# Kernel tuning notes

Hardware: AMD Instinct MI355X
Metric: run time of the kernel (lower is better)

Reference implementation:

```python
import jax, jax.numpy as jnp
import numpy as np

EPS = 1e-6
DN = ('NCHW', 'OIHW', 'NCHW')


def _dw_conv(s, w, dilation, k):
    pad = dilation * (k - 1) // 2
    return jax.lax.conv_general_dilated(
        s, w, window_strides=(1, 1), padding=[(pad, pad), (pad, pad)],
        rhs_dilation=(dilation, dilation), dimension_numbers=DN,
        feature_group_count=4)


def _branch(s, dw_w, pw_w, pw_b, dilation, k):
    h = _dw_conv(s, dw_w, dilation, k)           # [B,4,H,W]
    # pointwise 1x1 conv 4 -> 1
    return jnp.einsum('bchw,oc->bohw', h, pw_w) + pw_b[None, :, None, None]


def setup_inputs() -> dict:
    key = jax.random.key(0)
    ks = jax.random.split(key, 12)
    B, C, H, W = 32, 64, 128, 128
    nb, rh = 3, 8
    d = {}
    d['x'] = jax.random.normal(ks[0], (B, C, H, W), dtype=jnp.float32)
    # branch 0: k=3 d=1; branch 1: k=7 d=1; branch 2: k=7 d=2
    d['dw0'] = jax.random.normal(ks[1], (4, 1, 3, 3), dtype=jnp.float32) * 0.2
    d['dw1'] = jax.random.normal(ks[2], (4, 1, 7, 7), dtype=jnp.float32) * 0.1
    d['dw2'] = jax.random.normal(ks[3], (4, 1, 7, 7), dtype=jnp.float32) * 0.1
    d['pw0_w'] = jax.random.normal(ks[4], (1, 4), dtype=jnp.float32) * 0.5
    d['pw0_b'] = jnp.zeros((1,), dtype=jnp.float32)
    d['pw1_w'] = jax.random.normal(ks[5], (1, 4), dtype=jnp.float32) * 0.5
    d['pw1_b'] = jnp.zeros((1,), dtype=jnp.float32)
    d['pw2_w'] = jax.random.normal(ks[6], (1, 4), dtype=jnp.float32) * 0.5
    d['pw2_b'] = jnp.zeros((1,), dtype=jnp.float32)
    # router: 1x1 convs on pooled [B,4,1,1] == dense layers
    d['rw1'] = jax.random.normal(ks[7], (rh, 4), dtype=jnp.float32) * 0.5
    d['rb1'] = jnp.zeros((rh,), dtype=jnp.float32)
    d['rw2'] = jax.random.normal(ks[8], (nb, rh), dtype=jnp.float32) * 0.3
    d['rb2'] = jnp.zeros((nb,), dtype=jnp.float32)
    # t_raw = softplus_inverse(1.0)
    d['t_raw'] = jnp.asarray(np.log(np.expm1(1.0)), dtype=jnp.float32)
    return d


def reference(x, dw0, dw1, dw2, pw0_w, pw0_b, pw1_w, pw1_b, pw2_w, pw2_b,
              rw1, rb1, rw2, rb2, t_raw):
    B, C, H, W = x.shape
    avg_map = jnp.mean(x, axis=1, keepdims=True)        # [B,1,H,W]
    max_map = jnp.max(x, axis=1, keepdims=True)         # [B,1,H,W]
    xs = jnp.linspace(-1.0, 1.0, W, dtype=x.dtype)
    ys = jnp.linspace(-1.0, 1.0, H, dtype=x.dtype)
    yy, xx = jnp.meshgrid(ys, xs, indexing='ij')
    xg = jnp.broadcast_to(xx[None, None], (B, 1, H, W))
    yg = jnp.broadcast_to(yy[None, None], (B, 1, H, W))
    s = jnp.concatenate([avg_map, max_map, xg, yg], axis=1)  # [B,4,H,W]

    # router: global avg pool -> 1x1 conv -> relu -> 1x1 conv -> softmax
    pooled = jnp.mean(s, axis=(2, 3))                    # [B,4]
    hid = jax.nn.relu(pooled @ rw1.T + rb1)              # [B,rh]
    logits = hid @ rw2.T + rb2                           # [B,nb]
    rw = jax.nn.softmax(logits, axis=1)                  # [B,nb]

    z = jnp.stack([
        _branch(s, dw0, pw0_w, pw0_b, 1, 3),
        _branch(s, dw1, pw1_w, pw1_b, 1, 7),
        _branch(s, dw2, pw2_w, pw2_b, 2, 7),
    ], axis=1)                                           # [B,nb,1,H,W]

    wlogits = jnp.sum(rw[:, :, None, None, None] * z, axis=1)  # [B,1,H,W]
    T = jax.nn.softplus(t_raw) + EPS
    sa = jax.nn.sigmoid(wlogits / T)                     # [B,1,H,W]
    Y = x * sa                                           # [B,C,H,W]
    return (Y, sa)
```

## Files before the change

### kernel.cpp

```cpp
#include <hip/hip_runtime.h>

#define B_ 32
#define C_ 64
#define H_ 128
#define W_ 128
#define HW_ (H_*W_)
#define CHW_ (C_*HW_)

typedef float f4 __attribute__((ext_vector_type(4)));

__global__ __launch_bounds__(256) void k0_zpos(
    const float* __restrict__ dw0, const float* __restrict__ dw1,
    const float* __restrict__ dw2,
    const float* __restrict__ pw0w, const float* __restrict__ pw0b,
    const float* __restrict__ pw1w, const float* __restrict__ pw1b,
    const float* __restrict__ pw2w, const float* __restrict__ pw2b,
    float* __restrict__ zpos)
{
    int p = blockIdx.x * 256 + threadIdx.x;
    int gy = p >> 7, gx = p & 127;
    const float sc = 2.0f / 127.0f;
    float z0 = pw0b[0], z1 = pw1b[0], z2 = pw2b[0];
    float px0 = pw0w[2], py0 = pw0w[3];
    float px1 = pw1w[2], py1 = pw1w[3];
    float px2 = pw2w[2], py2 = pw2w[3];

    #pragma unroll
    for (int ky = 0; ky < 3; ++ky)
    #pragma unroll
    for (int kx = 0; kx < 3; ++kx) {
        int iy = gy + ky - 1, ix = gx + kx - 1;
        bool ok = ((unsigned)iy < H_) && ((unsigned)ix < W_);
        float xv = ok ? ix * sc - 1.0f : 0.0f;
        float yv = ok ? iy * sc - 1.0f : 0.0f;
        int t = ky * 3 + kx;
        z0 += px0 * dw0[18 + t] * xv + py0 * dw0[27 + t] * yv;
    }
    #pragma unroll
    for (int ky = 0; ky < 7; ++ky)
    #pragma unroll
    for (int kx = 0; kx < 7; ++kx) {
        int iy = gy + ky - 3, ix = gx + kx - 3;
        bool ok = ((unsigned)iy < H_) && ((unsigned)ix < W_);
        float xv = ok ? ix * sc - 1.0f : 0.0f;
        float yv = ok ? iy * sc - 1.0f : 0.0f;
        int t = ky * 7 + kx;
        z1 += px1 * dw1[98 + t] * xv + py1 * dw1[147 + t] * yv;
    }
    #pragma unroll
    for (int ky = 0; ky < 7; ++ky)
    #pragma unroll
    for (int kx = 0; kx < 7; ++kx) {
        int iy = gy + (ky - 3) * 2, ix = gx + (kx - 3) * 2;
        bool ok = ((unsigned)iy < H_) && ((unsigned)ix < W_);
        float xv = ok ? ix * sc - 1.0f : 0.0f;
        float yv = ok ? iy * sc - 1.0f : 0.0f;
        int t = ky * 7 + kx;
        z2 += px2 * dw2[98 + t] * xv + py2 * dw2[147 + t] * yv;
    }
    zpos[p]           = z0;
    zpos[HW_ + p]     = z1;
    zpos[2 * HW_ + p] = z2;
}

__global__ __launch_bounds__(256) void k1_reduce(
    const float* __restrict__ x, float* __restrict__ avgmap,
    float* __restrict__ maxmap, float* __restrict__ partial)
{
    int t = blockIdx.x * 256 + threadIdx.x;
    int base = t * 4;
    int b = base >> 14;
    int q = base & (HW_ - 1);
    const float4* xp = (const float4*)(x + (size_t)b * CHW_ + q);
    float4 v = xp[0];
    float4 s = v, m = v;
    #pragma unroll 8
    for (int c = 1; c < C_; ++c) {
        float4 u = xp[c * (HW_ / 4)];
        s.x += u.x; s.y += u.y; s.z += u.z; s.w += u.w;
        m.x = fmaxf(m.x, u.x); m.y = fmaxf(m.y, u.y);
        m.z = fmaxf(m.z, u.z); m.w = fmaxf(m.w, u.w);
    }
    const float inv = 1.0f / C_;
    float4 a = make_float4(s.x * inv, s.y * inv, s.z * inv, s.w * inv);
    ((float4*)avgmap)[t] = a;
    ((float4*)maxmap)[t] = m;

    float la = a.x + a.y + a.z + a.w;
    float lm = m.x + m.y + m.z + m.w;
    #pragma unroll
    for (int o = 32; o > 0; o >>= 1) {
        la += __shfl_down(la, o);
        lm += __shfl_down(lm, o);
    }
    __shared__ float wa[4], wm[4];
    int lane = threadIdx.x & 63, wid = threadIdx.x >> 6;
    if (lane == 0) { wa[wid] = la; wm[wid] = lm; }
    __syncthreads();
    if (threadIdx.x == 0) {
        partial[2 * blockIdx.x]     = wa[0] + wa[1] + wa[2] + wa[3];
        partial[2 * blockIdx.x + 1] = wm[0] + wm[1] + wm[2] + wm[3];
    }
}

__global__ void k2_router(const float* __restrict__ partial,
                          const float* __restrict__ rw1, const float* __restrict__ rb1,
                          const float* __restrict__ rw2, const float* __restrict__ rb2,
                          const float* __restrict__ t_raw,
                          float* __restrict__ rwout)
{
    int b = threadIdx.x;
    if (b >= B_) return;
    if (b == 0)
        rwout[96] = 1.0f / (log1pf(expf(t_raw[0])) + 1e-6f);
    float s0 = 0.0f, s1 = 0.0f;
    #pragma unroll
    for (int i = 0; i < 16; ++i) {
        s0 += partial[2 * (b * 16 + i)];
        s1 += partial[2 * (b * 16 + i) + 1];
    }
    float p0 = s0 * (1.0f / HW_);
    float p1 = s1 * (1.0f / HW_);
    float hid[8];
    #pragma unroll
    for (int j = 0; j < 8; ++j)
        hid[j] = fmaxf(0.0f, rb1[j] + rw1[j * 4] * p0 + rw1[j * 4 + 1] * p1);
    float lg[3];
    #pragma unroll
    for (int i = 0; i < 3; ++i) {
        float acc = rb2[i];
        #pragma unroll
        for (int j = 0; j < 8; ++j) acc += hid[j] * rw2[i * 8 + j];
        lg[i] = acc;
    }
    float mx = fmaxf(lg[0], fmaxf(lg[1], lg[2]));
    float e0 = expf(lg[0] - mx), e1 = expf(lg[1] - mx), e2 = expf(lg[2] - mx);
    float inv = 1.0f / (e0 + e1 + e2);
    rwout[b * 3 + 0] = e0 * inv;
    rwout[b * 3 + 1] = e1 * inv;
    rwout[b * 3 + 2] = e2 * inv;
}

__global__ __launch_bounds__(256) void k3_conv(
    const float* __restrict__ avgmap, const float* __restrict__ maxmap,
    const float* __restrict__ dw0, const float* __restrict__ dw1,
    const float* __restrict__ dw2,
    const float* __restrict__ pw0w, const float* __restrict__ pw1w,
    const float* __restrict__ pw2w,
    const float* __restrict__ zpos, const float* __restrict__ rw,
    float* __restrict__ sa_out)
{
    __shared__ float sA[14][140];
    __shared__ float sM[14][140];
    __shared__ float wA0[9], wM0[9];
    __shared__ float wA1[49], wM1[49], wA2[49], wM2[49];

    int b  = blockIdx.y;
    int y0 = blockIdx.x * 2;
    int tix = threadIdx.x;
    const float* am = avgmap + (size_t)b * HW_;
    const float* mm = maxmap + (size_t)b * HW_;

    for (int idx = tix; idx < 14 * 32; idx += 256) {
        int r = idx >> 5, c4 = idx & 31;
        int gy = y0 - 6 + r;
        bool ok = (unsigned)gy < H_;
        float4 av = ok ? ((const float4*)(am + gy * W_))[c4]
                       : make_float4(0.f, 0.f, 0.f, 0.f);
        float4 mv = ok ? ((const float4*)(mm + gy * W_))[c4]
                       : make_float4(0.f, 0.f, 0.f, 0.f);
        float* pa = &sA[r][6 + c4 * 4];
        float* pm = &sM[r][6 + c4 * 4];
        pa[0] = av.x; pa[1] = av.y; pa[2] = av.z; pa[3] = av.w;
        pm[0] = mv.x; pm[1] = mv.y; pm[2] = mv.z; pm[3] = mv.w;
    }
    for (int idx = tix; idx < 14 * 12; idx += 256) {
        int r = idx / 12, c = idx % 12;
        int cc = (c < 6) ? c : (134 + c - 6);
        sA[r][cc] = 0.0f;
        sM[r][cc] = 0.0f;
    }
    if (tix < 9)  { wA0[tix] = pw0w[0] * dw0[tix];
                    wM0[tix] = pw0w[1] * dw0[9 + tix]; }
    if (tix < 49) { wA1[tix] = pw1w[0] * dw1[tix];
                    wM1[tix] = pw1w[1] * dw1[49 + tix];
                    wA2[tix] = pw2w[0] * dw2[tix];
                    wM2[tix] = pw2w[1] * dw2[49 + tix]; }
    __syncthreads();

    int ly = tix >> 7;
    int lx = tix & 127;
    int gy = y0 + ly;
    int pidx = gy * W_ + lx;

    float z0 = zpos[pidx];
    float z1 = zpos[HW_ + pidx];
    float z2 = zpos[2 * HW_ + pidx];

    #pragma unroll
    for (int ky = 0; ky < 7; ++ky) {
        const float* ra = &sA[ly + 3 + ky][lx + 3];
        const float* rm = &sM[ly + 3 + ky][lx + 3];
        float av[7], mv[7];
        #pragma unroll
        for (int j = 0; j < 7; ++j) { av[j] = ra[j]; mv[j] = rm[j]; }
        #pragma unroll
        for (int j = 0; j < 7; ++j) {
            int t = ky * 7 + j;
            z1 += wA1[t] * av[j] + wM1[t] * mv[j];
        }
        if (ky >= 2 && ky <= 4) {
            #pragma unroll
            for (int j = 2; j <= 4; ++j) {
                int t = (ky - 2) * 3 + (j - 2);
                z0 += wA0[t] * av[j] + wM0[t] * mv[j];
            }
        }
    }
    #pragma unroll
    for (int ky = 0; ky < 7; ++ky) {
        const float* ra = &sA[ly + 2 * ky][lx];
        const float* rm = &sM[ly + 2 * ky][lx];
        #pragma unroll
        for (int kx = 0; kx < 7; ++kx) {
            int t = ky * 7 + kx;
            z2 += wA2[t] * ra[2 * kx] + wM2[t] * rm[2 * kx];
        }
    }

    float wl = rw[b * 3] * z0 + rw[b * 3 + 1] * z1 + rw[b * 3 + 2] * z2;
    float s = 1.0f / (1.0f + expf(-wl * rw[96]));
    sa_out[(size_t)b * HW_ + pidx] = s;
}

__global__ __launch_bounds__(256) void k4_apply(
    const float* __restrict__ x, const float* __restrict__ sa,
    float* __restrict__ y)
{
    int tile = blockIdx.x;
    int cg   = blockIdx.y;
    int b  = tile >> 4;
    int p4 = (tile & 15) * 256 + threadIdx.x;

    f4 sv = ((const f4*)(sa + (size_t)b * HW_))[p4];
    const f4* xb = (const f4*)(x + (size_t)b * CHW_) + p4;
    f4*       yb = (f4*)(y + (size_t)b * CHW_) + p4;

    #pragma unroll 4
    for (int k = 0; k < 16; ++k) {
        int c = cg * 16 + k;
        f4 v = xb[c * (HW_ / 4)];
        f4 r = v * sv;
        __builtin_nontemporal_store(r, &yb[c * (HW_ / 4)]);
    }
}

extern "C" void kernel_launch(void* const* d_in, const int* in_sizes, int n_in,
                              void* d_out, int out_size, void* d_ws, size_t ws_size,
                              hipStream_t stream)
{
    const float* x     = (const float*)d_in[0];
    const float* dw0   = (const float*)d_in[1];
    const float* dw1   = (const float*)d_in[2];
    const float* dw2   = (const float*)d_in[3];
    const float* pw0w  = (const float*)d_in[4];
    const float* pw0b  = (const float*)d_in[5];
    const float* pw1w  = (const float*)d_in[6];
    const float* pw1b  = (const float*)d_in[7];
    const float* pw2w  = (const float*)d_in[8];
    const float* pw2b  = (const float*)d_in[9];
    const float* rw1   = (const float*)d_in[10];
    const float* rb1   = (const float*)d_in[11];
    const float* rw2   = (const float*)d_in[12];
    const float* rb2   = (const float*)d_in[13];
    const float* t_raw = (const float*)d_in[14];

    float* ws      = (float*)d_ws;
    float* avgmap  = ws;
    float* maxmap  = ws + 524288;
    float* partial = ws + 1048576;
    float* rw      = ws + 1049600;
    float* zpos    = ws + 1049728;

    float* Y  = (float*)d_out;
    float* sa = Y + (size_t)B_ * CHW_;

    k0_zpos<<<HW_ / 256, 256, 0, stream>>>(
        dw0, dw1, dw2, pw0w, pw0b, pw1w, pw1b, pw2w, pw2b, zpos);
    k1_reduce<<<B_ * HW_ / 4 / 256, 256, 0, stream>>>(x, avgmap, maxmap, partial);
    k2_router<<<1, 64, 0, stream>>>(partial, rw1, rb1, rw2, rb2, t_raw, rw);

    dim3 g3(H_ / 2, B_);
    k3_conv<<<g3, 256, 0, stream>>>(
        avgmap, maxmap, dw0, dw1, dw2, pw0w, pw1w, pw2w, zpos, rw, sa);

    dim3 g4(B_ * HW_ / 4 / 256, 4);
    k4_apply<<<g4, 256, 0, stream>>>(x, sa, Y);
}
```

Before: 320.1 us.

## Fuse router, conv and apply kernels into one per-tile kernel

```diff
diff --git a/kernel.cpp b/kernel.cpp
--- a/kernel.cpp
+++ b/kernel.cpp
@@ -103,57 +103,26 @@
     }
 }
 
-__global__ void k2_router(const float* __restrict__ partial,
-                          const float* __restrict__ rw1, const float* __restrict__ rb1,
-                          const float* __restrict__ rw2, const float* __restrict__ rb2,
-                          const float* __restrict__ t_raw,
-                          float* __restrict__ rwout)
-{
-    int b = threadIdx.x;
-    if (b >= B_) return;
-    if (b == 0)
-        rwout[96] = 1.0f / (log1pf(expf(t_raw[0])) + 1e-6f);
-    float s0 = 0.0f, s1 = 0.0f;
-    #pragma unroll
-    for (int i = 0; i < 16; ++i) {
-        s0 += partial[2 * (b * 16 + i)];
-        s1 += partial[2 * (b * 16 + i) + 1];
-    }
-    float p0 = s0 * (1.0f / HW_);
-    float p1 = s1 * (1.0f / HW_);
-    float hid[8];
-    #pragma unroll
-    for (int j = 0; j < 8; ++j)
-        hid[j] = fmaxf(0.0f, rb1[j] + rw1[j * 4] * p0 + rw1[j * 4 + 1] * p1);
-    float lg[3];
-    #pragma unroll
-    for (int i = 0; i < 3; ++i) {
-        float acc = rb2[i];
-        #pragma unroll
-        for (int j = 0; j < 8; ++j) acc += hid[j] * rw2[i * 8 + j];
-        lg[i] = acc;
-    }
-    float mx = fmaxf(lg[0], fmaxf(lg[1], lg[2]));
-    float e0 = expf(lg[0] - mx), e1 = expf(lg[1] - mx), e2 = expf(lg[2] - mx);
-    float inv = 1.0f / (e0 + e1 + e2);
-    rwout[b * 3 + 0] = e0 * inv;
-    rwout[b * 3 + 1] = e1 * inv;
-    rwout[b * 3 + 2] = e2 * inv;
-}
-
-__global__ __launch_bounds__(256) void k3_conv(
+__global__ __launch_bounds__(256) void k34_fused(
+    const float* __restrict__ x,
     const float* __restrict__ avgmap, const float* __restrict__ maxmap,
     const float* __restrict__ dw0, const float* __restrict__ dw1,
     const float* __restrict__ dw2,
     const float* __restrict__ pw0w, const float* __restrict__ pw1w,
     const float* __restrict__ pw2w,
-    const float* __restrict__ zpos, const float* __restrict__ rw,
-    float* __restrict__ sa_out)
+    const float* __restrict__ zpos,
+    const float* __restrict__ partial,
+    const float* __restrict__ rw1, const float* __restrict__ rb1,
+    const float* __restrict__ rw2, const float* __restrict__ rb2,
+    const float* __restrict__ t_raw,
+    float* __restrict__ y, float* __restrict__ sa_out)
 {
     __shared__ float sA[14][140];
     __shared__ float sM[14][140];
     __shared__ float wA0[9], wM0[9];
     __shared__ float wA1[49], wM1[49], wA2[49], wM2[49];
+    __shared__ __align__(16) float ssa[256];
+    __shared__ float sRW[4];
 
     int b  = blockIdx.y;
     int y0 = blockIdx.x * 2;
@@ -186,6 +155,35 @@
                     wM1[tix] = pw1w[1] * dw1[49 + tix];
                     wA2[tix] = pw2w[0] * dw2[tix];
                     wM2[tix] = pw2w[1] * dw2[49 + tix]; }
+    if (tix == 0) {
+        float s0 = 0.0f, s1 = 0.0f;
+        #pragma unroll
+        for (int i = 0; i < 16; ++i) {
+            s0 += partial[2 * (b * 16 + i)];
+            s1 += partial[2 * (b * 16 + i) + 1];
+        }
+        float p0 = s0 * (1.0f / HW_);
+        float p1 = s1 * (1.0f / HW_);
+        float hid[8];
+        #pragma unroll
+        for (int j = 0; j < 8; ++j)
+            hid[j] = fmaxf(0.0f, rb1[j] + rw1[j * 4] * p0 + rw1[j * 4 + 1] * p1);
+        float lg[3];
+        #pragma unroll
+        for (int i = 0; i < 3; ++i) {
+            float acc = rb2[i];
+            #pragma unroll
+            for (int j = 0; j < 8; ++j) acc += hid[j] * rw2[i * 8 + j];
+            lg[i] = acc;
+        }
+        float mx = fmaxf(lg[0], fmaxf(lg[1], lg[2]));
+        float e0 = expf(lg[0] - mx), e1 = expf(lg[1] - mx), e2 = expf(lg[2] - mx);
+        float inv = 1.0f / (e0 + e1 + e2);
+        sRW[0] = e0 * inv;
+        sRW[1] = e1 * inv;
+        sRW[2] = e2 * inv;
+        sRW[3] = 1.0f / (log1pf(expf(t_raw[0])) + 1e-6f);
+    }
     __syncthreads();
 
     int ly = tix >> 7;
@@ -228,30 +226,23 @@
         }
     }
 
-    float wl = rw[b * 3] * z0 + rw[b * 3 + 1] * z1 + rw[b * 3 + 2] * z2;
-    float s = 1.0f / (1.0f + expf(-wl * rw[96]));
-    sa_out[(size_t)b * HW_ + pidx] = s;
-}
-
-__global__ __launch_bounds__(256) void k4_apply(
-    const float* __restrict__ x, const float* __restrict__ sa,
-    float* __restrict__ y)
-{
-    int tile = blockIdx.x;
-    int cg   = blockIdx.y;
-    int b  = tile >> 4;
-    int p4 = (tile & 15) * 256 + threadIdx.x;
-
-    f4 sv = ((const f4*)(sa + (size_t)b * HW_))[p4];
-    const f4* xb = (const f4*)(x + (size_t)b * CHW_) + p4;
-    f4*       yb = (f4*)(y + (size_t)b * CHW_) + p4;
-
+    float wl = sRW[0] * z0 + sRW[1] * z1 + sRW[2] * z2;
+    float s = 1.0f / (1.0f + expf(-wl * sRW[3]));
+    ssa[tix] = s;
+    __builtin_nontemporal_store(s, &sa_out[(size_t)b * HW_ + pidx]);
+    __syncthreads();
+
+    int wid  = tix >> 6;
+    int lane = tix & 63;
+    f4 sv = ((const f4*)ssa)[lane];
+    const float* xt = x + (size_t)b * CHW_ + y0 * W_;
+    float*       yt = y + (size_t)b * CHW_ + y0 * W_;
     #pragma unroll 4
     for (int k = 0; k < 16; ++k) {
-        int c = cg * 16 + k;
-        f4 v = xb[c * (HW_ / 4)];
-        f4 r = v * sv;
-        __builtin_nontemporal_store(r, &yb[c * (HW_ / 4)]);
+        int c = wid + k * 4;
+        f4 xv = *((const f4*)(xt + c * HW_) + lane);
+        f4 r  = xv * sv;
+        __builtin_nontemporal_store(r, (f4*)(yt + c * HW_) + lane);
     }
 }
 
@@ -279,8 +270,7 @@
     float* avgmap  = ws;
     float* maxmap  = ws + 524288;
     float* partial = ws + 1048576;
-    float* rw      = ws + 1049600;
-    float* zpos    = ws + 1049728;
+    float* zpos    = ws + 1049600;
 
     float* Y  = (float*)d_out;
     float* sa = Y + (size_t)B_ * CHW_;
@@ -288,12 +278,10 @@
     k0_zpos<<<HW_ / 256, 256, 0, stream>>>(
         dw0, dw1, dw2, pw0w, pw0b, pw1w, pw1b, pw2w, pw2b, zpos);
     k1_reduce<<<B_ * HW_ / 4 / 256, 256, 0, stream>>>(x, avgmap, maxmap, partial);
-    k2_router<<<1, 64, 0, stream>>>(partial, rw1, rb1, rw2, rb2, t_raw, rw);
-
-    dim3 g3(H_ / 2, B_);
-    k3_conv<<<g3, 256, 0, stream>>>(
-        avgmap, maxmap, dw0, dw1, dw2, pw0w, pw1w, pw2w, zpos, rw, sa);
-
-    dim3 g4(B_ * HW_ / 4 / 256, 4);
-    k4_apply<<<g4, 256, 0, stream>>>(x, sa, Y);
-}
+
+    dim3 g34(H_ / 2, B_);
+    k34_fused<<<g34, 256, 0, stream>>>(
+        x, avgmap, maxmap, dw0, dw1, dw2,
+        pw0w, pw1w, pw2w, zpos,
+        partial, rw1, rb1, rw2, rb2, t_raw, Y, sa);
+}
```

After: 295.0 us. 7.8% less time.
